# Kernel tuning notes

Hardware: AMD Instinct MI355X
Metric: run time of the kernel (lower is better)

## Reference

```python
import jax, jax.numpy as jnp
import numpy as np

NUM_EMBEDDINGS = 1024
EMBEDDING_DIM = 64
COMMITMENT_COST = 0.25


def setup_inputs() -> dict:
    key = jax.random.key(0)
    k1, k2 = jax.random.split(key)
    latents = jax.random.normal(k1, (64, EMBEDDING_DIM, 32, 32), dtype=jnp.float32)
    # torch init: uniform_(-1/num_embeddings, 1/num_embeddings)
    codebook = jax.random.uniform(
        k2, (NUM_EMBEDDINGS, EMBEDDING_DIM), dtype=jnp.float32,
        minval=-1.0 / NUM_EMBEDDINGS, maxval=1.0 / NUM_EMBEDDINGS)
    return {"latents": latents, "codebook": codebook}


def reference(latents, codebook):
    B, C, H, W = latents.shape
    K = codebook.shape[0]
    x = jnp.transpose(latents, (0, 2, 3, 1))            # [B,H,W,C]
    x_flat = x.reshape(-1, C)                            # [N,C]
    # squared euclidean distances [N,K]
    dist = (jnp.sum(x_flat ** 2, axis=1, keepdims=True)
            + jnp.sum(codebook ** 2, axis=1)
            - 2.0 * x_flat @ codebook.T)
    idx = jnp.argmin(dist, axis=1)                       # [N] int
    q_flat = codebook[idx]                               # [N,C]
    q = q_flat.reshape(x.shape)                          # [B,H,W,C]
    e_loss = jnp.mean((jax.lax.stop_gradient(q) - x) ** 2)
    q_loss = jnp.mean((q - jax.lax.stop_gradient(x)) ** 2)
    vq_loss = q_loss + COMMITMENT_COST * e_loss
    # straight-through estimator
    q_st = x + jax.lax.stop_gradient(q - x)
    quantized = jnp.transpose(q_st, (0, 3, 1, 2))        # [B,C,H,W]
    # perplexity from code usage histogram
    N = x_flat.shape[0]
    avg_probs = jnp.zeros((K,), dtype=jnp.float32).at[idx].add(1.0) / N
    perplexity = jnp.exp(-jnp.sum(avg_probs * jnp.log(avg_probs + 1e-10)))
    encoding_indices = idx.reshape(B, H, W)
    return (vq_loss, quantized, perplexity, encoding_indices)
```

## Files before the change

kernel.cpp:

```cpp
#include <hip/hip_runtime.h>

#define N_PTS   65536
#define K_CODES 1024
#define C_DIM   64
#define HW      1024
#define Q_ELEMS 4194304
#define NBLOCKS 1024

#define OUT_Q_OFF 1
#define OUT_P_OFF 4194305
#define OUT_I_OFF 4194306

#define WS_HIST 0
#define WS_CNT  4096
#define WS_SSE  4104
#define WS_CSUM 4112
#define WS_CBP  8208

#define EPS_A_W 7.5e-5f
#define EPS_T_W 2.0e-4f

typedef float f32x16 __attribute__((ext_vector_type(16)));
typedef short bf16x8 __attribute__((ext_vector_type(8)));

__device__ __forceinline__ unsigned short bf16rn(float f) {
    unsigned int u = __float_as_uint(f);
    return (unsigned short)((u + 0x7FFFu + ((u >> 16) & 1u)) >> 16);
}
__device__ __forceinline__ float bf16tof(unsigned short h) {
    return __uint_as_float(((unsigned int)h) << 16);
}

__device__ __forceinline__ float np_pairwise_sumsq64(const float* a) {
    float r[8];
    #pragma unroll
    for (int j = 0; j < 8; ++j) r[j] = __fmul_rn(a[j], a[j]);
    #pragma unroll
    for (int i = 8; i < 64; i += 8) {
        #pragma unroll
        for (int j = 0; j < 8; ++j)
            r[j] = __fadd_rn(r[j], __fmul_rn(a[i + j], a[i + j]));
    }
    return __fadd_rn(__fadd_rn(__fadd_rn(r[0], r[1]), __fadd_rn(r[2], r[3])),
                     __fadd_rn(__fadd_rn(r[4], r[5]), __fadd_rn(r[6], r[7])));
}

__global__ void vq_prep(const float* __restrict__ cb, float* __restrict__ csum,
                        unsigned short* __restrict__ cbp,
                        unsigned int* __restrict__ hist,
                        unsigned int* __restrict__ counter,
                        double* __restrict__ sse) {
    __shared__ float rs[32 * 65];
    __shared__ float csl[32];
    const int t = blockIdx.x, tid = threadIdx.x;
    if (tid < 32) hist[t * 32 + tid] = 0u;
    if (t == 0 && tid == 0) { *counter = 0u; *sse = 0.0; }
    const float* src = cb + (size_t)t * 2048;
    for (int i = tid; i < 2048; i += 256) {
        int row = i >> 6, d = i & 63;
        rs[row * 65 + d] = src[i];
    }
    __syncthreads();
    if (tid < 32) {
        float cs = np_pairwise_sumsq64(&rs[tid * 65]);
        csum[t * 32 + tid] = cs;
        csl[tid] = cs;
    }
    __syncthreads();
    if (tid < 64) {
        int l31 = tid & 31, half = tid >> 5;
        const float* r = &rs[l31 * 65];
        unsigned short* dst = cbp + (size_t)t * 9 * 512;
        #pragma unroll
        for (int c = 0; c < 4; ++c) {
            bf16x8 h8, l8;
            #pragma unroll
            for (int j = 0; j < 8; ++j) {
                float f = r[c * 16 + half * 8 + j];
                unsigned short h = bf16rn(f);
                h8[j] = (short)h;
                l8[j] = (short)bf16rn(f - bf16tof(h));
            }
            *(bf16x8*)(dst + (size_t)(c * 2 + 0) * 512 + tid * 8) = h8;
            *(bf16x8*)(dst + (size_t)(c * 2 + 1) * 512 + tid * 8) = l8;
        }
        bf16x8 c8;
        #pragma unroll
        for (int j = 0; j < 8; ++j) c8[j] = 0;
        if (half == 0) c8[0] = (short)bf16rn(-0.5f * csl[l31]);
        *(bf16x8*)(dst + (size_t)8 * 512 + tid * 8) = c8;
    }
}

__global__ __launch_bounds__(256, 2) void vq_main(
        const float* __restrict__ latents,
        const float* __restrict__ cb,
        const float* __restrict__ csum,
        const unsigned short* __restrict__ cbp,
        unsigned int* __restrict__ hist,
        double* __restrict__ sse,
        unsigned int* __restrict__ counter,
        float* __restrict__ out) {
    __shared__ float xs[64 * 65];
    __shared__ float tmax[32 * 64];
    __shared__ float sm1[2][64], sm2[2][64];
    __shared__ int   si1[2][64];
    __shared__ float m1f[64];
    __shared__ int   fk[64], ambig[64];
    __shared__ int   acount, lastflag;
    __shared__ double red[256];

    const int tid  = threadIdx.x;
    const int lane = tid & 63, wave = tid >> 6;
    const int chh = wave & 1, pg = wave >> 1;
    const int n0 = blockIdx.x * 64;
    const int b = n0 >> 10, hw0 = n0 & 1023;
    const float* xg = latents + (size_t)b * C_DIM * HW + hw0;

    for (int i = tid; i < 64 * 64; i += 256) {
        int p = i & 63, d = i >> 6;
        xs[p * 65 + d] = xg[(size_t)d * HW + p];
    }
    if (tid == 0) acount = 0;
    __syncthreads();

    const int l31 = lane & 31, half = lane >> 5;
    const int pb = (pg << 5) + l31;
    bf16x8 xh[4], xl[4], x4;
    #pragma unroll
    for (int c = 0; c < 4; ++c)
        #pragma unroll
        for (int j = 0; j < 8; ++j) {
            float f = xs[pb * 65 + c * 16 + half * 8 + j];
            unsigned short h = bf16rn(f);
            xh[c][j] = (short)h;
            xl[c][j] = (short)bf16rn(f - bf16tof(h));
        }
    #pragma unroll
    for (int j = 0; j < 8; ++j) x4[j] = 0;
    if (half == 0) x4[0] = (short)0x3F80;

    float m1 = -3e38f, m2 = -3e38f;
    int i1 = 0;
    const int RC[16] = {0,1,2,3,8,9,10,11,16,17,18,19,24,25,26,27};
    const int rh4 = half * 4;

    for (int t = 0; t < 16; ++t) {
        const int tg = (chh << 4) + t;
        const bf16x8* bp = (const bf16x8*)cbp + (size_t)tg * 576 + lane;
        bf16x8 ch[4], cl[4], ca;
        #pragma unroll
        for (int c = 0; c < 4; ++c) {
            ch[c] = bp[c * 128];
            cl[c] = bp[c * 128 + 64];
        }
        ca = bp[512];
        f32x16 accA, accB1, accB2;
        #pragma unroll
        for (int r = 0; r < 16; ++r) { accA[r] = 0.0f; accB1[r] = 0.0f; accB2[r] = 0.0f; }
        #pragma unroll
        for (int c = 0; c < 4; ++c)
            accA = __builtin_amdgcn_mfma_f32_32x32x16_bf16(ch[c], xh[c], accA, 0, 0, 0);
        accA = __builtin_amdgcn_mfma_f32_32x32x16_bf16(ca, x4, accA, 0, 0, 0);
        #pragma unroll
        for (int c = 0; c < 4; ++c)
            accB1 = __builtin_amdgcn_mfma_f32_32x32x16_bf16(ch[c], xl[c], accB1, 0, 0, 0);
        #pragma unroll
        for (int c = 0; c < 4; ++c)
            accB2 = __builtin_amdgcn_mfma_f32_32x32x16_bf16(cl[c], xh[c], accB2, 0, 0, 0);
        float tl = -3e38f;
        const int tb2 = tg << 5;
        #pragma unroll
        for (int r = 0; r < 16; ++r) {
            float v = __fadd_rn(__fadd_rn(accA[r], accB1[r]), accB2[r]);
            int k = tb2 + RC[r] + rh4;
            m2 = fmaxf(m2, fminf(m1, v));
            i1 = (v > m1) ? k : i1;
            m1 = fmaxf(m1, v);
            tl = fmaxf(tl, v);
        }
        tl = fmaxf(tl, __shfl_xor(tl, 32, 64));
        if (half == 0) tmax[tg * 64 + pb] = tl;
    }
    {
        float m1o = __shfl_xor(m1, 32, 64);
        float m2o = __shfl_xor(m2, 32, 64);
        int   i1o = __shfl_xor(i1, 32, 64);
        m2 = fmaxf(fmaxf(m2, m2o), fminf(m1, m1o));
        i1 = (m1o > m1) ? i1o : i1;
        m1 = fmaxf(m1, m1o);
        if (half == 0) { sm1[chh][pb] = m1; sm2[chh][pb] = m2; si1[chh][pb] = i1; }
    }
    __syncthreads();

    if (tid < 64) {
        float a1 = sm1[0][tid], a2 = sm2[0][tid];
        float b1 = sm1[1][tid], b2 = sm2[1][tid];
        float mm1 = fmaxf(a1, b1);
        float mm2 = fmaxf(fminf(a1, b1), fmaxf(a2, b2));
        m1f[tid] = mm1;
        fk[tid] = (b1 > a1) ? si1[1][tid] : si1[0][tid];
        if (mm2 >= mm1 - EPS_A_W) {
            int a = atomicAdd(&acount, 1);
            ambig[a] = tid;
        }
    }
    __syncthreads();

    for (int a = wave; a < acount; a += 4) {
        int p = ambig[a];
        const float* xrow = &xs[p * 65];
        float Aq = np_pairwise_sumsq64(xrow);
        float thr = m1f[p] - EPS_T_W;
        unsigned long long best = ~0ULL;
        for (int t = 0; t < 32; ++t) {
            if (tmax[t * 64 + p] < thr) continue;
            if (lane < 32) {
                int k = (t << 5) + lane;
                const float* crow = cb + (size_t)k * 64;
                float m = 0.0f;
                #pragma unroll
                for (int d = 0; d < 64; ++d) m = __fmaf_rn(xrow[d], crow[d], m);
                float D = __fsub_rn(__fadd_rn(Aq, csum[k]), __fmul_rn(2.0f, m));
                unsigned long long key =
                    ((unsigned long long)__float_as_uint(D) << 10) | (unsigned)k;
                best = (key < best) ? key : best;
            }
        }
        #pragma unroll
        for (int off = 32; off > 0; off >>= 1) {
            unsigned long long o = __shfl_xor(best, off, 64);
            best = (o < best) ? o : best;
        }
        if (lane == 0) fk[p] = (int)(best & 1023ULL);
    }
    __syncthreads();

    if (tid < 64) {
        out[OUT_I_OFF + n0 + tid] = (float)fk[tid];
        atomicAdd(&hist[fk[tid]], 1u);
    }

    {
        double e = 0.0;
        #pragma unroll
        for (int it = 0; it < 16; ++it) {
            int i = tid + it * 256;
            int p = i >> 6, c = i & 63;
            float q = cb[(size_t)fk[p] * 64 + c];
            float xv = xs[p * 65 + c];
            double df = (double)xv - (double)q;
            e = fma(df, df, e);
            xs[p * 65 + c] = q;
        }
        red[tid] = e;
    }
    __syncthreads();
    if (tid < 128) red[tid] += red[tid + 128];
    __syncthreads();
    if (tid < 64) {
        double v = red[tid] + red[tid + 64];
        #pragma unroll
        for (int off = 32; off > 0; off >>= 1) v += __shfl_down(v, off, 64);
        if (tid == 0) atomicAdd(sse, v);
    }
    #pragma unroll
    for (int it = 0; it < 16; ++it) {
        int i = tid + it * 256;
        int p = i & 63, c = i >> 6;
        out[OUT_Q_OFF + (size_t)b * 65536 + (size_t)c * HW + hw0 + p] = xs[p * 65 + c];
    }

    __syncthreads();
    if (tid == 0) lastflag = (atomicAdd(counter, 1u) == NBLOCKS - 1) ? 1 : 0;
    __syncthreads();
    if (lastflag) {
        double s = 0.0;
        for (int i = tid; i < K_CODES; i += 256) {
            double p = (double)atomicAdd(&hist[i], 0u) / (double)N_PTS;
            s += p * log(p + 1e-10);
        }
        red[tid] = s;
        __syncthreads();
        for (int w = 128; w > 0; w >>= 1) {
            if (tid < w) red[tid] += red[tid + w];
            __syncthreads();
        }
        if (tid == 0) {
            out[OUT_P_OFF] = (float)exp(-red[0]);
            double sv = atomicAdd(sse, 0.0);
            out[0] = (float)(1.25 * sv / (double)Q_ELEMS);
        }
    }
}

extern "C" void kernel_launch(void* const* d_in, const int* in_sizes, int n_in,
                              void* d_out, int out_size, void* d_ws, size_t ws_size,
                              hipStream_t stream) {
    const float* latents = (const float*)d_in[0];
    const float* cb      = (const float*)d_in[1];
    float* out = (float*)d_out;
    char* ws = (char*)d_ws;

    unsigned int*   hist    = (unsigned int*)(ws + WS_HIST);
    unsigned int*   counter = (unsigned int*)(ws + WS_CNT);
    double*         sse     = (double*)(ws + WS_SSE);
    float*          csum    = (float*)(ws + WS_CSUM);
    unsigned short* cbp     = (unsigned short*)(ws + WS_CBP);

    vq_prep <<<32, 256, 0, stream>>>(cb, csum, cbp, hist, counter, sse);
    vq_main <<<NBLOCKS, 256, 0, stream>>>(latents, cb, csum, cbp, hist, sse, counter, out);
}
```

Before: 152.4 us.

## Process 128 points per block with full-codebook waves and register double-buffered tiles

Each block now handles 128 points instead of 64, and each wave scans all 32 codebook tiles for its own 32 points, so the cross-wave merge of half-codebook minima through shared memory and a barrier goes away. Codebook tile loads are double-buffered in registers to overlap global loads with MFMA work, and the argmin tracking is split into two independent chains to shorten dependency chains. Ambiguous-point rescoring is done per wave using a ballot mask instead of a shared atomic list. The trade-offs are higher register pressure, more shared memory, and half as many blocks, which may reduce occupancy and load balance.

```diff
diff --git a/kernel.cpp b/kernel.cpp
--- a/kernel.cpp
+++ b/kernel.cpp
@@ -5,7 +5,7 @@
 #define C_DIM   64
 #define HW      1024
 #define Q_ELEMS 4194304
-#define NBLOCKS 1024
+#define NBLOCKS 512
 
 #define OUT_Q_OFF 1
 #define OUT_P_OFF 4194305
@@ -101,31 +101,26 @@
         double* __restrict__ sse,
         unsigned int* __restrict__ counter,
         float* __restrict__ out) {
-    __shared__ float xs[64 * 65];
-    __shared__ float tmax[32 * 64];
-    __shared__ float sm1[2][64], sm2[2][64];
-    __shared__ int   si1[2][64];
-    __shared__ float m1f[64];
-    __shared__ int   fk[64], ambig[64];
-    __shared__ int   acount, lastflag;
+    __shared__ float xs[128 * 65];
+    __shared__ float tmax[32 * 128];
+    __shared__ int   fk[128];
+    __shared__ int   lastflag;
     __shared__ double red[256];
 
     const int tid  = threadIdx.x;
     const int lane = tid & 63, wave = tid >> 6;
-    const int chh = wave & 1, pg = wave >> 1;
-    const int n0 = blockIdx.x * 64;
+    const int n0 = blockIdx.x * 128;
     const int b = n0 >> 10, hw0 = n0 & 1023;
     const float* xg = latents + (size_t)b * C_DIM * HW + hw0;
 
-    for (int i = tid; i < 64 * 64; i += 256) {
-        int p = i & 63, d = i >> 6;
+    for (int i = tid; i < 128 * 64; i += 256) {
+        int p = i & 127, d = i >> 7;
         xs[p * 65 + d] = xg[(size_t)d * HW + p];
     }
-    if (tid == 0) acount = 0;
     __syncthreads();
 
     const int l31 = lane & 31, half = lane >> 5;
-    const int pb = (pg << 5) + l31;
+    const int pb = (wave << 5) + l31;
     bf16x8 xh[4], xl[4], x4;
     #pragma unroll
     for (int c = 0; c < 4; ++c)
@@ -140,21 +135,22 @@
     for (int j = 0; j < 8; ++j) x4[j] = 0;
     if (half == 0) x4[0] = (short)0x3F80;
 
-    float m1 = -3e38f, m2 = -3e38f;
-    int i1 = 0;
+    float m1a = -3e38f, m2a = -3e38f, m1b = -3e38f, m2b = -3e38f;
+    int i1a = 0, i1b = 0;
     const int RC[16] = {0,1,2,3,8,9,10,11,16,17,18,19,24,25,26,27};
     const int rh4 = half * 4;
-
-    for (int t = 0; t < 16; ++t) {
-        const int tg = (chh << 4) + t;
-        const bf16x8* bp = (const bf16x8*)cbp + (size_t)tg * 576 + lane;
-        bf16x8 ch[4], cl[4], ca;
+    const bf16x8* base = (const bf16x8*)cbp;
+
+    auto load_tile = [&](int t, bf16x8* ch, bf16x8* cl, bf16x8& ca) {
+        const bf16x8* bp = base + (size_t)t * 576 + lane;
         #pragma unroll
         for (int c = 0; c < 4; ++c) {
             ch[c] = bp[c * 128];
             cl[c] = bp[c * 128 + 64];
         }
         ca = bp[512];
+    };
+    auto screen_tile = [&](int t, const bf16x8* ch, const bf16x8* cl, bf16x8 ca) {
         f32x16 accA, accB1, accB2;
         #pragma unroll
         for (int r = 0; r < 16; ++r) { accA[r] = 0.0f; accB1[r] = 0.0f; accB2[r] = 0.0f; }
@@ -168,75 +164,89 @@
         #pragma unroll
         for (int c = 0; c < 4; ++c)
             accB2 = __builtin_amdgcn_mfma_f32_32x32x16_bf16(cl[c], xh[c], accB2, 0, 0, 0);
-        float tl = -3e38f;
-        const int tb2 = tg << 5;
-        #pragma unroll
-        for (int r = 0; r < 16; ++r) {
+        const int tb2 = t << 5;
+        float tla = -3e38f, tlb = -3e38f;
+        #pragma unroll
+        for (int r = 0; r < 8; ++r) {
             float v = __fadd_rn(__fadd_rn(accA[r], accB1[r]), accB2[r]);
             int k = tb2 + RC[r] + rh4;
-            m2 = fmaxf(m2, fminf(m1, v));
-            i1 = (v > m1) ? k : i1;
-            m1 = fmaxf(m1, v);
-            tl = fmaxf(tl, v);
-        }
+            m2a = fmaxf(m2a, fminf(m1a, v));
+            i1a = (v > m1a) ? k : i1a;
+            m1a = fmaxf(m1a, v);
+            tla = fmaxf(tla, v);
+        }
+        #pragma unroll
+        for (int r = 8; r < 16; ++r) {
+            float v = __fadd_rn(__fadd_rn(accA[r], accB1[r]), accB2[r]);
+            int k = tb2 + RC[r] + rh4;
+            m2b = fmaxf(m2b, fminf(m1b, v));
+            i1b = (v > m1b) ? k : i1b;
+            m1b = fmaxf(m1b, v);
+            tlb = fmaxf(tlb, v);
+        }
+        float tl = fmaxf(tla, tlb);
         tl = fmaxf(tl, __shfl_xor(tl, 32, 64));
-        if (half == 0) tmax[tg * 64 + pb] = tl;
-    }
+        if (half == 0) tmax[t * 128 + pb] = tl;
+    };
+
+    bf16x8 chA[4], clA[4], caA, chB[4], clB[4], caB;
+    load_tile(0, chA, clA, caA);
+    for (int t = 0; t < 32; t += 2) {
+        load_tile(t + 1, chB, clB, caB);
+        screen_tile(t, chA, clA, caA);
+        if (t + 2 < 32) load_tile(t + 2, chA, clA, caA);
+        screen_tile(t + 1, chB, clB, caB);
+    }
+
+    float m1 = fmaxf(m1a, m1b);
+    float m2 = fmaxf(fmaxf(m2a, m2b), fminf(m1a, m1b));
+    int i1 = (m1b > m1a || (m1b == m1a && i1b < i1a)) ? i1b : i1a;
     {
         float m1o = __shfl_xor(m1, 32, 64);
         float m2o = __shfl_xor(m2, 32, 64);
         int   i1o = __shfl_xor(i1, 32, 64);
         m2 = fmaxf(fmaxf(m2, m2o), fminf(m1, m1o));
-        i1 = (m1o > m1) ? i1o : i1;
+        i1 = (m1o > m1 || (m1o == m1 && i1o < i1)) ? i1o : i1;
         m1 = fmaxf(m1, m1o);
-        if (half == 0) { sm1[chh][pb] = m1; sm2[chh][pb] = m2; si1[chh][pb] = i1; }
-    }
-    __syncthreads();
-
-    if (tid < 64) {
-        float a1 = sm1[0][tid], a2 = sm2[0][tid];
-        float b1 = sm1[1][tid], b2 = sm2[1][tid];
-        float mm1 = fmaxf(a1, b1);
-        float mm2 = fmaxf(fminf(a1, b1), fmaxf(a2, b2));
-        m1f[tid] = mm1;
-        fk[tid] = (b1 > a1) ? si1[1][tid] : si1[0][tid];
-        if (mm2 >= mm1 - EPS_A_W) {
-            int a = atomicAdd(&acount, 1);
-            ambig[a] = tid;
-        }
-    }
-    __syncthreads();
-
-    for (int a = wave; a < acount; a += 4) {
-        int p = ambig[a];
-        const float* xrow = &xs[p * 65];
-        float Aq = np_pairwise_sumsq64(xrow);
-        float thr = m1f[p] - EPS_T_W;
-        unsigned long long best = ~0ULL;
-        for (int t = 0; t < 32; ++t) {
-            if (tmax[t * 64 + p] < thr) continue;
-            if (lane < 32) {
-                int k = (t << 5) + lane;
-                const float* crow = cb + (size_t)k * 64;
-                float m = 0.0f;
-                #pragma unroll
-                for (int d = 0; d < 64; ++d) m = __fmaf_rn(xrow[d], crow[d], m);
-                float D = __fsub_rn(__fadd_rn(Aq, csum[k]), __fmul_rn(2.0f, m));
-                unsigned long long key =
-                    ((unsigned long long)__float_as_uint(D) << 10) | (unsigned)k;
-                best = (key < best) ? key : best;
+        if (half == 0) fk[pb] = i1;
+    }
+
+    {
+        bool amb = (half == 0) && (m2 >= m1 - EPS_A_W);
+        unsigned long long mask = __ballot(amb);
+        while (mask) {
+            int lp = __ffsll(mask) - 1;
+            mask &= mask - 1;
+            int p = (wave << 5) + lp;
+            float thr = __shfl(m1, lp, 64) - EPS_T_W;
+            const float* xrow = &xs[p * 65];
+            float Aq = np_pairwise_sumsq64(xrow);
+            unsigned long long best = ~0ULL;
+            for (int t = 0; t < 32; ++t) {
+                if (tmax[t * 128 + p] < thr) continue;
+                if (lane < 32) {
+                    int k = (t << 5) + lane;
+                    const float* crow = cb + (size_t)k * 64;
+                    float m = 0.0f;
+                    #pragma unroll
+                    for (int d = 0; d < 64; ++d) m = __fmaf_rn(xrow[d], crow[d], m);
+                    float D = __fsub_rn(__fadd_rn(Aq, csum[k]), __fmul_rn(2.0f, m));
+                    unsigned long long key =
+                        ((unsigned long long)__float_as_uint(D) << 10) | (unsigned)k;
+                    best = (key < best) ? key : best;
+                }
             }
-        }
-        #pragma unroll
-        for (int off = 32; off > 0; off >>= 1) {
-            unsigned long long o = __shfl_xor(best, off, 64);
-            best = (o < best) ? o : best;
-        }
-        if (lane == 0) fk[p] = (int)(best & 1023ULL);
-    }
-    __syncthreads();
-
-    if (tid < 64) {
+            #pragma unroll
+            for (int off = 32; off > 0; off >>= 1) {
+                unsigned long long o = __shfl_xor(best, off, 64);
+                best = (o < best) ? o : best;
+            }
+            if (lane == 0) fk[p] = (int)(best & 1023ULL);
+        }
+    }
+    __syncthreads();
+
+    if (tid < 128) {
         out[OUT_I_OFF + n0 + tid] = (float)fk[tid];
         atomicAdd(&hist[fk[tid]], 1u);
     }
@@ -244,7 +254,7 @@
     {
         double e = 0.0;
         #pragma unroll
-        for (int it = 0; it < 16; ++it) {
+        for (int it = 0; it < 32; ++it) {
             int i = tid + it * 256;
             int p = i >> 6, c = i & 63;
             float q = cb[(size_t)fk[p] * 64 + c];
@@ -265,9 +275,9 @@
         if (tid == 0) atomicAdd(sse, v);
     }
     #pragma unroll
-    for (int it = 0; it < 16; ++it) {
+    for (int it = 0; it < 32; ++it) {
         int i = tid + it * 256;
-        int p = i & 63, c = i >> 6;
+        int p = i & 127, c = i >> 7;
         out[OUT_Q_OFF + (size_t)b * 65536 + (size_t)c * HW + hw0 + p] = xs[p * 65 + c];
     }
 
```

After: 147.9 us. 1.03x faster.
